# Kernel tuning notes

Measured on AMD Instinct MI355X. Metric: run time of the kernel, lower is better.

## Reference

```python
import jax, jax.numpy as jnp
import numpy as np

SESSION_CHANNELS = [128, 160, 192, 224, 240, 248, 252, 256]  # per-session channel counts
N_SESS = len(SESSION_CHANNELS)
B, MAX_C, MAX_T = 16, 256, 4096
HID, N_SRC = 512, 256


def setup_inputs() -> dict:
    key = jax.random.key(0)
    ks = jax.random.split(key, 7)
    session_ids = jax.random.randint(ks[0], (B,), 0, N_SESS)
    chan_table = jnp.asarray(SESSION_CHANNELS)
    channel_counts = chan_table[session_ids]
    seq_lens = jax.random.randint(ks[1], (B,), MAX_T // 2, MAX_T + 1)
    x = jax.random.normal(ks[2], (B, MAX_C, MAX_T), jnp.float32)
    # zero-pad beyond true channels and true time (as the docstring states)
    cmask = (jnp.arange(MAX_C)[None, :] < channel_counts[:, None]).astype(x.dtype)
    tmask = (jnp.arange(MAX_T)[None, :] < seq_lens[:, None]).astype(x.dtype)
    x = x * cmask[:, :, None] * tmask[:, None, :]
    # per-session Linear(num_channels -> HID), padded to MAX_C rows (torch-style uniform init)
    lim1 = 1.0 / np.sqrt(MAX_C)
    W_sess = jax.random.uniform(ks[3], (N_SESS, MAX_C, HID), jnp.float32, -lim1, lim1)
    b_sess = jax.random.uniform(ks[4], (N_SESS, HID), jnp.float32, -lim1, lim1)
    lim2 = 1.0 / np.sqrt(HID)
    W2 = jax.random.uniform(ks[5], (HID, N_SRC), jnp.float32, -lim2, lim2)
    b2 = jax.random.uniform(ks[6], (N_SRC,), jnp.float32, -lim2, lim2)
    return dict(x=x, session_ids=session_ids, channel_counts=channel_counts,
                seq_lens=seq_lens, W_sess=W_sess, b_sess=b_sess, W2=W2, b2=b2)


def reference(x, session_ids, channel_counts, seq_lens, W_sess, b_sess, W2, b2):
    # mask padded channels so the full-width contraction equals the sliced per-sample matmul
    cmask = (jnp.arange(x.shape[1])[None, :] < channel_counts[:, None]).astype(x.dtype)
    xm = x * cmask[:, :, None]                       # (B, Max_C, Max_T)
    W = W_sess[session_ids]                          # (B, Max_C, HID) gathered per sample
    b = b_sess[session_ids]                          # (B, HID)
    h = jnp.einsum('bct,bch->bht', xm, W) + b[:, :, None]
    h = jax.nn.gelu(h, approximate=False)            # torch nn.GELU default is exact erf
    out = jnp.einsum('bht,hs->bst', h, W2) + b2[None, :, None]  # (B, N_SRC, Max_T)
    tmask = (jnp.arange(x.shape[2])[None, :] < seq_lens[:, None]).astype(x.dtype)
    return out * tmask[:, None, :]
```

## Files before the change

### kernel.cpp

```cpp
#include <hip/hip_runtime.h>

typedef __attribute__((ext_vector_type(8))) _Float16 f16x8;
typedef __attribute__((ext_vector_type(4))) _Float16 f16x4;
typedef __attribute__((ext_vector_type(4))) float f32x4;

#define NB 16
#define MAXC 256
#define MAXT 4096
#define HID 512
#define NSRC 256
#define TT 64

__device__ __forceinline__ float gelu_fast(float x) {
  float p = x * x;
  float q = __builtin_fmaf(p, -0.10294336f, -2.30220778f);
  float e = __builtin_amdgcn_exp2f(x * q);
  return x * __builtin_amdgcn_rcpf(1.0f + e);
}

__global__ void transpose_cvt_kernel(const float* __restrict__ src,
                                     _Float16* __restrict__ dst, int R, int C) {
  __shared__ float tile[32][33];
  const float* s = src + (size_t)blockIdx.z * R * C;
  _Float16* d = dst + (size_t)blockIdx.z * R * C;
  int c0 = blockIdx.x * 32, r0 = blockIdx.y * 32;
  int tx = threadIdx.x, ty = threadIdx.y;
  for (int i = ty; i < 32; i += 8)
    tile[i][tx] = s[(size_t)(r0 + i) * C + (c0 + tx)];
  __syncthreads();
  for (int i = ty; i < 32; i += 8)
    d[(size_t)(c0 + i) * R + (r0 + tx)] = (_Float16)tile[tx][i];
}

__global__ __launch_bounds__(512, 4)
void fused_sess_proj_kernel(const float* __restrict__ x,
                            const int* __restrict__ sess_ids,
                            const int* __restrict__ seq_lens,
                            const _Float16* __restrict__ W1t,
                            const float* __restrict__ b_sess,
                            const _Float16* __restrict__ W2t,
                            const float* __restrict__ b2,
                            float* __restrict__ out) {
  int wg = blockIdx.x;
  int b = wg >> 6;
  int t0 = (wg & 63) * TT;
  int seqlen = seq_lens[b];
  int tid = threadIdx.x;

  if (t0 >= seqlen) {
    int row = tid >> 1;
    int part = tid & 1;
    float* po = out + ((size_t)b * NSRC + row) * MAXT + t0 + part * 32;
    f32x4 z = {0.f, 0.f, 0.f, 0.f};
    #pragma unroll
    for (int i = 0; i < 8; ++i) *(f32x4*)(po + i * 4) = z;
    return;
  }

  __shared__ _Float16 Xs[TT * MAXC];
  __shared__ _Float16 Hs[TT * 256];

  {
    int c = tid & 255;
    int th = tid >> 8;
    const float* xp = x + ((size_t)b * MAXC + c) * MAXT + t0 + th * 32;
    #pragma unroll
    for (int i = 0; i < 8; ++i) {
      f32x4 v = *(const f32x4*)(xp + i * 4);
      #pragma unroll
      for (int k = 0; k < 4; ++k) {
        int t = th * 32 + i * 4 + k;
        Xs[t * 256 + (c ^ ((t & 7) << 3))] = (_Float16)v[k];
      }
    }
  }
  __syncthreads();

  int lane = tid & 63;
  int w = tid >> 6;
  int lg = lane >> 4;
  int lr = lane & 15;
  int sid = sess_ids[b];
  const _Float16* W1s = W1t + (size_t)sid * HID * MAXC;

  f32x4 acc2[2][4];
  #pragma unroll
  for (int mi = 0; mi < 2; ++mi) {
    f32x4 bv = *(const f32x4*)(b2 + w * 32 + mi * 16 + lg * 4);
    #pragma unroll
    for (int ni = 0; ni < 4; ++ni) acc2[mi][ni] = bv;
  }

  #pragma unroll
  for (int ch = 0; ch < 2; ++ch) {
    f32x4 acc1[2][4];
    #pragma unroll
    for (int mi = 0; mi < 2; ++mi) {
      f32x4 bv = *(const f32x4*)(b_sess + sid * HID + ch * 256 + w * 32 + mi * 16 + lg * 4);
      #pragma unroll
      for (int ni = 0; ni < 4; ++ni) acc1[mi][ni] = bv;
    }
    #pragma unroll
    for (int ks = 0; ks < 8; ++ks) {
      int k0 = ks * 32;
      f16x8 af[2], bf[4];
      #pragma unroll
      for (int mi = 0; mi < 2; ++mi)
        af[mi] = *(const f16x8*)(W1s +
            (size_t)(ch * 256 + w * 32 + mi * 16 + lr) * MAXC + k0 + lg * 8);
      #pragma unroll
      for (int ni = 0; ni < 4; ++ni) {
        int t = ni * 16 + lr;
        bf[ni] = *(const f16x8*)(&Xs[t * 256 + ((k0 + lg * 8) ^ ((t & 7) << 3))]);
      }
      #pragma unroll
      for (int mi = 0; mi < 2; ++mi)
        #pragma unroll
        for (int ni = 0; ni < 4; ++ni)
          acc1[mi][ni] = __builtin_amdgcn_mfma_f32_16x16x32_f16(af[mi], bf[ni], acc1[mi][ni], 0, 0, 0);
    }
    #pragma unroll
    for (int mi = 0; mi < 2; ++mi) {
      int hh = w * 32 + mi * 16 + lg * 4;
      #pragma unroll
      for (int ni = 0; ni < 4; ++ni) {
        int t = ni * 16 + lr;
        f16x4 g;
        #pragma unroll
        for (int r = 0; r < 4; ++r) g[r] = (_Float16)gelu_fast(acc1[mi][ni][r]);
        *(f16x4*)(&Hs[t * 256 + (hh ^ ((t & 7) << 3))]) = g;
      }
    }
    __syncthreads();
    #pragma unroll
    for (int ks = 0; ks < 8; ++ks) {
      int k0 = ks * 32;
      f16x8 af[2], bf[4];
      #pragma unroll
      for (int mi = 0; mi < 2; ++mi)
        af[mi] = *(const f16x8*)(W2t +
            (size_t)(w * 32 + mi * 16 + lr) * HID + ch * 256 + k0 + lg * 8);
      #pragma unroll
      for (int ni = 0; ni < 4; ++ni) {
        int t = ni * 16 + lr;
        bf[ni] = *(const f16x8*)(&Hs[t * 256 + ((k0 + lg * 8) ^ ((t & 7) << 3))]);
      }
      #pragma unroll
      for (int mi = 0; mi < 2; ++mi)
        #pragma unroll
        for (int ni = 0; ni < 4; ++ni)
          acc2[mi][ni] = __builtin_amdgcn_mfma_f32_16x16x32_f16(af[mi], bf[ni], acc2[mi][ni], 0, 0, 0);
    }
    __syncthreads();
  }

  #pragma unroll
  for (int mi = 0; mi < 2; ++mi) {
    int s0 = w * 32 + mi * 16 + lg * 4;
    #pragma unroll
    for (int ni = 0; ni < 4; ++ni) {
      int t = t0 + ni * 16 + lr;
      float m = (t < seqlen) ? 1.0f : 0.0f;
      #pragma unroll
      for (int r = 0; r < 4; ++r)
        out[((size_t)b * NSRC + s0 + r) * MAXT + t] = acc2[mi][ni][r] * m;
    }
  }
}

extern "C" void kernel_launch(void* const* d_in, const int* in_sizes, int n_in,
                              void* d_out, int out_size, void* d_ws, size_t ws_size,
                              hipStream_t stream) {
  const float* x      = (const float*)d_in[0];
  const int* sess     = (const int*)d_in[1];
  const int* seq      = (const int*)d_in[3];
  const float* W_sess = (const float*)d_in[4];
  const float* b_sess = (const float*)d_in[5];
  const float* W2     = (const float*)d_in[6];
  const float* b2     = (const float*)d_in[7];
  float* out = (float*)d_out;

  _Float16* W1t = (_Float16*)d_ws;
  _Float16* W2t = (_Float16*)((char*)d_ws + (size_t)8 * HID * MAXC * sizeof(_Float16));

  dim3 tb(32, 8);
  transpose_cvt_kernel<<<dim3(HID / 32, MAXC / 32, 8), tb, 0, stream>>>(W_sess, W1t, MAXC, HID);
  transpose_cvt_kernel<<<dim3(NSRC / 32, HID / 32, 1), tb, 0, stream>>>(W2, W2t, HID, NSRC);

  fused_sess_proj_kernel<<<dim3(NB * (MAXT / TT)), dim3(512), 0, stream>>>(
      x, sess, seq, W1t, b_sess, W2t, b2, out);
}
```

Baseline: 90.30 us.

## Preload weight fragments into registers and interleave GEMM stages with double-buffered H

Holds all W1 and W2 A-fragments for the current half in registers, issuing those loads before the x tile staging. The next half's fragments are loaded while the current MFMAs run. The second half of GEMM1 is interleaved with the first half of GEMM2 using a double-buffered Hs, which removes one barrier and hides global weight latency. The cost is much higher register pressure (launch bounds lowered to 2 blocks per SM, with 64 extra VGPRs of fragments) and double the LDS for Hs, which cuts occupancy.

```diff
diff --git a/kernel.cpp b/kernel.cpp
--- a/kernel.cpp
+++ b/kernel.cpp
@@ -32,7 +32,7 @@
     d[(size_t)(c0 + i) * R + (r0 + tx)] = (_Float16)tile[tx][i];
 }
 
-__global__ __launch_bounds__(512, 4)
+__global__ __launch_bounds__(512, 2)
 void fused_sess_proj_kernel(const float* __restrict__ x,
                             const int* __restrict__ sess_ids,
                             const int* __restrict__ seq_lens,
@@ -58,23 +58,7 @@
   }
 
   __shared__ _Float16 Xs[TT * MAXC];
-  __shared__ _Float16 Hs[TT * 256];
-
-  {
-    int c = tid & 255;
-    int th = tid >> 8;
-    const float* xp = x + ((size_t)b * MAXC + c) * MAXT + t0 + th * 32;
-    #pragma unroll
-    for (int i = 0; i < 8; ++i) {
-      f32x4 v = *(const f32x4*)(xp + i * 4);
-      #pragma unroll
-      for (int k = 0; k < 4; ++k) {
-        int t = th * 32 + i * 4 + k;
-        Xs[t * 256 + (c ^ ((t & 7) << 3))] = (_Float16)v[k];
-      }
-    }
-  }
-  __syncthreads();
+  __shared__ _Float16 Hs[2][TT * 256];
 
   int lane = tid & 63;
   int w = tid >> 6;
@@ -83,31 +67,107 @@
   int sid = sess_ids[b];
   const _Float16* W1s = W1t + (size_t)sid * HID * MAXC;
 
-  f32x4 acc2[2][4];
-  #pragma unroll
-  for (int mi = 0; mi < 2; ++mi) {
-    f32x4 bv = *(const f32x4*)(b2 + w * 32 + mi * 16 + lg * 4);
-    #pragma unroll
-    for (int ni = 0; ni < 4; ++ni) acc2[mi][ni] = bv;
-  }
-
-  #pragma unroll
-  for (int ch = 0; ch < 2; ++ch) {
-    f32x4 acc1[2][4];
+  f16x8 AF1[8][2];
+  f16x8 AF2[8][2];
+  #pragma unroll
+  for (int ks = 0; ks < 8; ++ks)
     #pragma unroll
     for (int mi = 0; mi < 2; ++mi) {
-      f32x4 bv = *(const f32x4*)(b_sess + sid * HID + ch * 256 + w * 32 + mi * 16 + lg * 4);
-      #pragma unroll
-      for (int ni = 0; ni < 4; ++ni) acc1[mi][ni] = bv;
-    }
-    #pragma unroll
-    for (int ks = 0; ks < 8; ++ks) {
-      int k0 = ks * 32;
-      f16x8 af[2], bf[4];
+      AF1[ks][mi] = *(const f16x8*)(W1s +
+          (size_t)(w * 32 + mi * 16 + lr) * MAXC + ks * 32 + lg * 8);
+      AF2[ks][mi] = *(const f16x8*)(W2t +
+          (size_t)(w * 32 + mi * 16 + lr) * HID + ks * 32 + lg * 8);
+    }
+
+  {
+    int c = tid & 255;
+    int th = tid >> 8;
+    const float* xp = x + ((size_t)b * MAXC + c) * MAXT + t0 + th * 32;
+    #pragma unroll
+    for (int i = 0; i < 8; ++i) {
+      f32x4 v = *(const f32x4*)(xp + i * 4);
+      #pragma unroll
+      for (int k = 0; k < 4; ++k) {
+        int t = th * 32 + i * 4 + k;
+        Xs[t * 256 + (c ^ ((t & 7) << 3))] = (_Float16)v[k];
+      }
+    }
+  }
+
+  f32x4 acc2[2][4], acc1[2][4];
+  #pragma unroll
+  for (int mi = 0; mi < 2; ++mi) {
+    f32x4 bv2 = *(const f32x4*)(b2 + w * 32 + mi * 16 + lg * 4);
+    f32x4 bv1 = *(const f32x4*)(b_sess + sid * HID + w * 32 + mi * 16 + lg * 4);
+    #pragma unroll
+    for (int ni = 0; ni < 4; ++ni) { acc2[mi][ni] = bv2; acc1[mi][ni] = bv1; }
+  }
+
+  __syncthreads();
+
+  #pragma unroll
+  for (int ks = 0; ks < 8; ++ks) {
+    int k0 = ks * 32;
+    f16x8 bf[4];
+    #pragma unroll
+    for (int ni = 0; ni < 4; ++ni) {
+      int t = ni * 16 + lr;
+      bf[ni] = *(const f16x8*)(&Xs[t * 256 + ((k0 + lg * 8) ^ ((t & 7) << 3))]);
+    }
+    #pragma unroll
+    for (int mi = 0; mi < 2; ++mi)
+      #pragma unroll
+      for (int ni = 0; ni < 4; ++ni)
+        acc1[mi][ni] = __builtin_amdgcn_mfma_f32_16x16x32_f16(AF1[ks][mi], bf[ni], acc1[mi][ni], 0, 0, 0);
+    #pragma unroll
+    for (int mi = 0; mi < 2; ++mi)
+      AF1[ks][mi] = *(const f16x8*)(W1s +
+          (size_t)(256 + w * 32 + mi * 16 + lr) * MAXC + k0 + lg * 8);
+  }
+
+  #pragma unroll
+  for (int mi = 0; mi < 2; ++mi) {
+    int hh = w * 32 + mi * 16 + lg * 4;
+    #pragma unroll
+    for (int ni = 0; ni < 4; ++ni) {
+      int t = ni * 16 + lr;
+      f16x4 g;
+      #pragma unroll
+      for (int r = 0; r < 4; ++r) g[r] = (_Float16)gelu_fast(acc1[mi][ni][r]);
+      *(f16x4*)(&Hs[0][t * 256 + (hh ^ ((t & 7) << 3))]) = g;
+    }
+  }
+  #pragma unroll
+  for (int mi = 0; mi < 2; ++mi) {
+    f32x4 bv1 = *(const f32x4*)(b_sess + sid * HID + 256 + w * 32 + mi * 16 + lg * 4);
+    #pragma unroll
+    for (int ni = 0; ni < 4; ++ni) acc1[mi][ni] = bv1;
+  }
+
+  __syncthreads();
+
+  #pragma unroll
+  for (int ks = 0; ks < 8; ++ks) {
+    int k0 = ks * 32;
+    {
+      f16x8 bf[4];
+      #pragma unroll
+      for (int ni = 0; ni < 4; ++ni) {
+        int t = ni * 16 + lr;
+        bf[ni] = *(const f16x8*)(&Hs[0][t * 256 + ((k0 + lg * 8) ^ ((t & 7) << 3))]);
+      }
       #pragma unroll
       for (int mi = 0; mi < 2; ++mi)
-        af[mi] = *(const f16x8*)(W1s +
-            (size_t)(ch * 256 + w * 32 + mi * 16 + lr) * MAXC + k0 + lg * 8);
+        #pragma unroll
+        for (int ni = 0; ni < 4; ++ni)
+          acc2[mi][ni] = __builtin_amdgcn_mfma_f32_16x16x32_f16(AF2[ks][mi], bf[ni], acc2[mi][ni], 0, 0, 0);
+    }
+    #pragma unroll
+    for (int mi = 0; mi < 2; ++mi)
+      AF2[ks][mi] = *(const f16x8*)(W2t +
+          (size_t)(w * 32 + mi * 16 + lr) * HID + 256 + k0 + lg * 8);
+    {
+      f16x8 bf[4];
       #pragma unroll
       for (int ni = 0; ni < 4; ++ni) {
         int t = ni * 16 + lr;
@@ -117,41 +177,39 @@
       for (int mi = 0; mi < 2; ++mi)
         #pragma unroll
         for (int ni = 0; ni < 4; ++ni)
-          acc1[mi][ni] = __builtin_amdgcn_mfma_f32_16x16x32_f16(af[mi], bf[ni], acc1[mi][ni], 0, 0, 0);
-    }
-    #pragma unroll
-    for (int mi = 0; mi < 2; ++mi) {
-      int hh = w * 32 + mi * 16 + lg * 4;
-      #pragma unroll
-      for (int ni = 0; ni < 4; ++ni) {
-        int t = ni * 16 + lr;
-        f16x4 g;
-        #pragma unroll
-        for (int r = 0; r < 4; ++r) g[r] = (_Float16)gelu_fast(acc1[mi][ni][r]);
-        *(f16x4*)(&Hs[t * 256 + (hh ^ ((t & 7) << 3))]) = g;
-      }
-    }
-    __syncthreads();
-    #pragma unroll
-    for (int ks = 0; ks < 8; ++ks) {
-      int k0 = ks * 32;
-      f16x8 af[2], bf[4];
-      #pragma unroll
-      for (int mi = 0; mi < 2; ++mi)
-        af[mi] = *(const f16x8*)(W2t +
-            (size_t)(w * 32 + mi * 16 + lr) * HID + ch * 256 + k0 + lg * 8);
-      #pragma unroll
-      for (int ni = 0; ni < 4; ++ni) {
-        int t = ni * 16 + lr;
-        bf[ni] = *(const f16x8*)(&Hs[t * 256 + ((k0 + lg * 8) ^ ((t & 7) << 3))]);
-      }
-      #pragma unroll
-      for (int mi = 0; mi < 2; ++mi)
-        #pragma unroll
-        for (int ni = 0; ni < 4; ++ni)
-          acc2[mi][ni] = __builtin_amdgcn_mfma_f32_16x16x32_f16(af[mi], bf[ni], acc2[mi][ni], 0, 0, 0);
-    }
-    __syncthreads();
+          acc1[mi][ni] = __builtin_amdgcn_mfma_f32_16x16x32_f16(AF1[ks][mi], bf[ni], acc1[mi][ni], 0, 0, 0);
+    }
+  }
+
+  #pragma unroll
+  for (int mi = 0; mi < 2; ++mi) {
+    int hh = w * 32 + mi * 16 + lg * 4;
+    #pragma unroll
+    for (int ni = 0; ni < 4; ++ni) {
+      int t = ni * 16 + lr;
+      f16x4 g;
+      #pragma unroll
+      for (int r = 0; r < 4; ++r) g[r] = (_Float16)gelu_fast(acc1[mi][ni][r]);
+      *(f16x4*)(&Hs[1][t * 256 + (hh ^ ((t & 7) << 3))]) = g;
+    }
+  }
+
+  __syncthreads();
+
+  #pragma unroll
+  for (int ks = 0; ks < 8; ++ks) {
+    int k0 = ks * 32;
+    f16x8 bf[4];
+    #pragma unroll
+    for (int ni = 0; ni < 4; ++ni) {
+      int t = ni * 16 + lr;
+      bf[ni] = *(const f16x8*)(&Hs[1][t * 256 + ((k0 + lg * 8) ^ ((t & 7) << 3))]);
+    }
+    #pragma unroll
+    for (int mi = 0; mi < 2; ++mi)
+      #pragma unroll
+      for (int ni = 0; ni < 4; ++ni)
+        acc2[mi][ni] = __builtin_amdgcn_mfma_f32_16x16x32_f16(AF2[ks][mi], bf[ni], acc2[mi][ni], 0, 0, 0);
   }
 
   #pragma unroll
```

New measurement: 96.91 us. 1.07x slower.

## Double-buffer weight fragments in registers and restructure phases with lightweight barriers

Applied to the files above, without the earlier changes.

Unrolls the two hidden-dimension chunks into explicit phases. Each phase prefetches the next two k-steps of weight fragments into a register double buffer, so global weight loads overlap with MFMA work, and MFMA blocks are wrapped in s_setprio. Full __syncthreads are replaced by an inline-asm LDS-wait-plus-barrier. The second chunk's bias loads and weight prefetch are issued before the barrier. The x staging now has each thread load two channel rows and write packed fp16 pairs with cvt_pkrtz, which rounds toward zero instead of to nearest and so slightly changes numerics.

```diff
diff --git a/kernel.cpp b/kernel.cpp
--- a/kernel.cpp
+++ b/kernel.cpp
@@ -2,6 +2,7 @@
 
 typedef __attribute__((ext_vector_type(8))) _Float16 f16x8;
 typedef __attribute__((ext_vector_type(4))) _Float16 f16x4;
+typedef __attribute__((ext_vector_type(2))) __fp16 fp16v2;
 typedef __attribute__((ext_vector_type(4))) float f32x4;
 
 #define NB 16
@@ -10,6 +11,8 @@
 #define HID 512
 #define NSRC 256
 #define TT 64
+
+#define BAR() asm volatile("s_waitcnt lgkmcnt(0)\n\ts_barrier" ::: "memory")
 
 __device__ __forceinline__ float gelu_fast(float x) {
   float p = x * x;
@@ -31,6 +34,38 @@
   for (int i = ty; i < 32; i += 8)
     d[(size_t)(c0 + i) * R + (r0 + tx)] = (_Float16)tile[tx][i];
 }
+
+#define A1ADDR(mi, ks) (W1s + (size_t)(chbase + w * 32 + (mi)*16 + lr) * MAXC + (ks)*32 + lg * 8)
+#define A2ADDR(mi, ks) (W2t + (size_t)(w * 32 + (mi)*16 + lr) * HID + chbase + (ks)*32 + lg * 8)
+
+#define PREFETCH(AADDR)                          \
+  AF[0][0] = *(const f16x8*)AADDR(0, 0);         \
+  AF[0][1] = *(const f16x8*)AADDR(1, 0);         \
+  AF[1][0] = *(const f16x8*)AADDR(0, 1);         \
+  AF[1][1] = *(const f16x8*)AADDR(1, 1);
+
+#define RUN_PHASE(AADDR, BS, ACC)                                              \
+  _Pragma("unroll")                                                            \
+  for (int ks = 0; ks < 8; ++ks) {                                             \
+    f16x8 a0 = AF[ks & 1][0], a1 = AF[ks & 1][1];                              \
+    if (ks < 6) {                                                              \
+      AF[ks & 1][0] = *(const f16x8*)AADDR(0, ks + 2);                         \
+      AF[ks & 1][1] = *(const f16x8*)AADDR(1, ks + 2);                         \
+    }                                                                          \
+    f16x8 bf[4];                                                               \
+    _Pragma("unroll")                                                          \
+    for (int ni = 0; ni < 4; ++ni) {                                           \
+      int t = ni * 16 + lr;                                                    \
+      bf[ni] = *(const f16x8*)(&BS[t * 256 + ((ks * 32 + lg * 8) ^ ((t & 7) << 3))]); \
+    }                                                                          \
+    __builtin_amdgcn_s_setprio(1);                                             \
+    _Pragma("unroll")                                                          \
+    for (int ni = 0; ni < 4; ++ni) {                                           \
+      ACC[0][ni] = __builtin_amdgcn_mfma_f32_16x16x32_f16(a0, bf[ni], ACC[0][ni], 0, 0, 0); \
+      ACC[1][ni] = __builtin_amdgcn_mfma_f32_16x16x32_f16(a1, bf[ni], ACC[1][ni], 0, 0, 0); \
+    }                                                                          \
+    __builtin_amdgcn_s_setprio(0);                                             \
+  }
 
 __global__ __launch_bounds__(512, 4)
 void fused_sess_proj_kernel(const float* __restrict__ x,
@@ -60,22 +95,6 @@
   __shared__ _Float16 Xs[TT * MAXC];
   __shared__ _Float16 Hs[TT * 256];
 
-  {
-    int c = tid & 255;
-    int th = tid >> 8;
-    const float* xp = x + ((size_t)b * MAXC + c) * MAXT + t0 + th * 32;
-    #pragma unroll
-    for (int i = 0; i < 8; ++i) {
-      f32x4 v = *(const f32x4*)(xp + i * 4);
-      #pragma unroll
-      for (int k = 0; k < 4; ++k) {
-        int t = th * 32 + i * 4 + k;
-        Xs[t * 256 + (c ^ ((t & 7) << 3))] = (_Float16)v[k];
-      }
-    }
-  }
-  __syncthreads();
-
   int lane = tid & 63;
   int w = tid >> 6;
   int lg = lane >> 4;
@@ -83,76 +102,87 @@
   int sid = sess_ids[b];
   const _Float16* W1s = W1t + (size_t)sid * HID * MAXC;
 
-  f32x4 acc2[2][4];
-  #pragma unroll
-  for (int mi = 0; mi < 2; ++mi) {
-    f32x4 bv = *(const f32x4*)(b2 + w * 32 + mi * 16 + lg * 4);
-    #pragma unroll
-    for (int ni = 0; ni < 4; ++ni) acc2[mi][ni] = bv;
-  }
-
-  #pragma unroll
-  for (int ch = 0; ch < 2; ++ch) {
-    f32x4 acc1[2][4];
-    #pragma unroll
-    for (int mi = 0; mi < 2; ++mi) {
-      f32x4 bv = *(const f32x4*)(b_sess + sid * HID + ch * 256 + w * 32 + mi * 16 + lg * 4);
+  {
+    int c2 = (tid & 127) * 2;
+    int th = tid >> 7;
+    const float* xp = x + ((size_t)b * MAXC + c2) * MAXT + t0 + th * 16;
+    f32x4 va[4], vb[4];
+    #pragma unroll
+    for (int i = 0; i < 4; ++i) va[i] = *(const f32x4*)(xp + i * 4);
+    #pragma unroll
+    for (int i = 0; i < 4; ++i) vb[i] = *(const f32x4*)(xp + MAXT + i * 4);
+    #pragma unroll
+    for (int k = 0; k < 16; ++k) {
+      int t = th * 16 + k;
+      fp16v2 p = __builtin_amdgcn_cvt_pkrtz(va[k >> 2][k & 3], vb[k >> 2][k & 3]);
+      *(fp16v2*)(&Xs[t * 256 + (c2 ^ ((t & 7) << 3))]) = p;
+    }
+  }
+
+  f16x8 AF[2][2];
+  int chbase = 0;
+  PREFETCH(A1ADDR);
+
+  f32x4 acc2[2][4], acc1[2][4];
+  #pragma unroll
+  for (int mi = 0; mi < 2; ++mi) {
+    f32x4 bv2 = *(const f32x4*)(b2 + w * 32 + mi * 16 + lg * 4);
+    f32x4 bv1 = *(const f32x4*)(b_sess + sid * HID + w * 32 + mi * 16 + lg * 4);
+    #pragma unroll
+    for (int ni = 0; ni < 4; ++ni) { acc2[mi][ni] = bv2; acc1[mi][ni] = bv1; }
+  }
+
+  BAR();
+
+  RUN_PHASE(A1ADDR, Xs, acc1);
+
+  #pragma unroll
+  for (int mi = 0; mi < 2; ++mi) {
+    int hh = w * 32 + mi * 16 + lg * 4;
+    #pragma unroll
+    for (int ni = 0; ni < 4; ++ni) {
+      int t = ni * 16 + lr;
+      f16x4 g;
       #pragma unroll
-      for (int ni = 0; ni < 4; ++ni) acc1[mi][ni] = bv;
-    }
-    #pragma unroll
-    for (int ks = 0; ks < 8; ++ks) {
-      int k0 = ks * 32;
-      f16x8 af[2], bf[4];
+      for (int r = 0; r < 4; ++r) g[r] = (_Float16)gelu_fast(acc1[mi][ni][r]);
+      *(f16x4*)(&Hs[t * 256 + (hh ^ ((t & 7) << 3))]) = g;
+    }
+  }
+  #pragma unroll
+  for (int mi = 0; mi < 2; ++mi) {
+    f32x4 bv1 = *(const f32x4*)(b_sess + sid * HID + 256 + w * 32 + mi * 16 + lg * 4);
+    #pragma unroll
+    for (int ni = 0; ni < 4; ++ni) acc1[mi][ni] = bv1;
+  }
+
+  PREFETCH(A2ADDR);
+  BAR();
+
+  RUN_PHASE(A2ADDR, Hs, acc2);
+
+  chbase = 256;
+  PREFETCH(A1ADDR);
+  BAR();
+
+  RUN_PHASE(A1ADDR, Xs, acc1);
+
+  #pragma unroll
+  for (int mi = 0; mi < 2; ++mi) {
+    int hh = w * 32 + mi * 16 + lg * 4;
+    #pragma unroll
+    for (int ni = 0; ni < 4; ++ni) {
+      int t = ni * 16 + lr;
+      f16x4 g;
       #pragma unroll
-      for (int mi = 0; mi < 2; ++mi)
-        af[mi] = *(const f16x8*)(W1s +
-            (size_t)(ch * 256 + w * 32 + mi * 16 + lr) * MAXC + k0 + lg * 8);
-      #pragma unroll
-      for (int ni = 0; ni < 4; ++ni) {
-        int t = ni * 16 + lr;
-        bf[ni] = *(const f16x8*)(&Xs[t * 256 + ((k0 + lg * 8) ^ ((t & 7) << 3))]);
-      }
-      #pragma unroll
-      for (int mi = 0; mi < 2; ++mi)
-        #pragma unroll
-        for (int ni = 0; ni < 4; ++ni)
-          acc1[mi][ni] = __builtin_amdgcn_mfma_f32_16x16x32_f16(af[mi], bf[ni], acc1[mi][ni], 0, 0, 0);
-    }
-    #pragma unroll
-    for (int mi = 0; mi < 2; ++mi) {
-      int hh = w * 32 + mi * 16 + lg * 4;
-      #pragma unroll
-      for (int ni = 0; ni < 4; ++ni) {
-        int t = ni * 16 + lr;
-        f16x4 g;
-        #pragma unroll
-        for (int r = 0; r < 4; ++r) g[r] = (_Float16)gelu_fast(acc1[mi][ni][r]);
-        *(f16x4*)(&Hs[t * 256 + (hh ^ ((t & 7) << 3))]) = g;
-      }
-    }
-    __syncthreads();
-    #pragma unroll
-    for (int ks = 0; ks < 8; ++ks) {
-      int k0 = ks * 32;
-      f16x8 af[2], bf[4];
-      #pragma unroll
-      for (int mi = 0; mi < 2; ++mi)
-        af[mi] = *(const f16x8*)(W2t +
-            (size_t)(w * 32 + mi * 16 + lr) * HID + ch * 256 + k0 + lg * 8);
-      #pragma unroll
-      for (int ni = 0; ni < 4; ++ni) {
-        int t = ni * 16 + lr;
-        bf[ni] = *(const f16x8*)(&Hs[t * 256 + ((k0 + lg * 8) ^ ((t & 7) << 3))]);
-      }
-      #pragma unroll
-      for (int mi = 0; mi < 2; ++mi)
-        #pragma unroll
-        for (int ni = 0; ni < 4; ++ni)
-          acc2[mi][ni] = __builtin_amdgcn_mfma_f32_16x16x32_f16(af[mi], bf[ni], acc2[mi][ni], 0, 0, 0);
-    }
-    __syncthreads();
-  }
+      for (int r = 0; r < 4; ++r) g[r] = (_Float16)gelu_fast(acc1[mi][ni][r]);
+      *(f16x4*)(&Hs[t * 256 + (hh ^ ((t & 7) << 3))]) = g;
+    }
+  }
+
+  PREFETCH(A2ADDR);
+  BAR();
+
+  RUN_PHASE(A2ADDR, Hs, acc2);
 
   #pragma unroll
   for (int mi = 0; mi < 2; ++mi) {
```

Result: slower. 94.37 us (+4.5%).

## Make fused kernel persistent over four time tiles with prefetched x and weights

Applied to the files above, without the earlier changes.

Each workgroup now handles four consecutive 64-step time tiles, so the grid shrinks to 256 blocks. The next tile's x values are prefetched into registers while the current one is computed. Weight fragments are double-buffered from global memory. The full 512-wide hidden tile is kept in LDS, so the two hidden chunks and their extra barriers go away, and wave tiling is changed (4x4 for GEMM1, 4x2 for GEMM2). This aims to hide global load latency and cut per-block overhead, at the cost of more LDS and registers, lower occupancy, and fewer blocks to balance across CUs.

```diff
diff --git a/kernel.cpp b/kernel.cpp
--- a/kernel.cpp
+++ b/kernel.cpp
@@ -2,6 +2,7 @@
 
 typedef __attribute__((ext_vector_type(8))) _Float16 f16x8;
 typedef __attribute__((ext_vector_type(4))) _Float16 f16x4;
+typedef __attribute__((ext_vector_type(2))) __fp16 fp16v2;
 typedef __attribute__((ext_vector_type(4))) float f32x4;
 
 #define NB 16
@@ -10,6 +11,10 @@
 #define HID 512
 #define NSRC 256
 #define TT 64
+
+#define BAR() asm volatile("s_waitcnt lgkmcnt(0)\n\ts_barrier" ::: "memory")
+
+#define MFMA(a, b, c) __builtin_amdgcn_mfma_f32_16x16x32_f16(a, b, c, 0, 0, 0)
 
 __device__ __forceinline__ float gelu_fast(float x) {
   float p = x * x;
@@ -32,7 +37,7 @@
     d[(size_t)(c0 + i) * R + (r0 + tx)] = (_Float16)tile[tx][i];
 }
 
-__global__ __launch_bounds__(512, 4)
+__global__ __launch_bounds__(512, 2)
 void fused_sess_proj_kernel(const float* __restrict__ x,
                             const int* __restrict__ sess_ids,
                             const int* __restrict__ seq_lens,
@@ -41,129 +46,169 @@
                             const _Float16* __restrict__ W2t,
                             const float* __restrict__ b2,
                             float* __restrict__ out) {
-  int wg = blockIdx.x;
-  int b = wg >> 6;
-  int t0 = (wg & 63) * TT;
+  int g = blockIdx.x;
+  int b = g >> 4;
+  int tile0 = (g & 15) * 4;
   int seqlen = seq_lens[b];
+  int sid = sess_ids[b];
   int tid = threadIdx.x;
-
-  if (t0 >= seqlen) {
-    int row = tid >> 1;
-    int part = tid & 1;
-    float* po = out + ((size_t)b * NSRC + row) * MAXT + t0 + part * 32;
-    f32x4 z = {0.f, 0.f, 0.f, 0.f};
-    #pragma unroll
-    for (int i = 0; i < 8; ++i) *(f32x4*)(po + i * 4) = z;
-    return;
-  }
-
-  __shared__ _Float16 Xs[TT * MAXC];
-  __shared__ _Float16 Hs[TT * 256];
-
-  {
-    int c = tid & 255;
-    int th = tid >> 8;
-    const float* xp = x + ((size_t)b * MAXC + c) * MAXT + t0 + th * 32;
-    #pragma unroll
-    for (int i = 0; i < 8; ++i) {
-      f32x4 v = *(const f32x4*)(xp + i * 4);
-      #pragma unroll
-      for (int k = 0; k < 4; ++k) {
-        int t = th * 32 + i * 4 + k;
-        Xs[t * 256 + (c ^ ((t & 7) << 3))] = (_Float16)v[k];
-      }
-    }
-  }
-  __syncthreads();
-
   int lane = tid & 63;
   int w = tid >> 6;
   int lg = lane >> 4;
   int lr = lane & 15;
-  int sid = sess_ids[b];
+  int sb = w >> 1;
+  int tb = w & 1;
   const _Float16* W1s = W1t + (size_t)sid * HID * MAXC;
 
-  f32x4 acc2[2][4];
-  #pragma unroll
-  for (int mi = 0; mi < 2; ++mi) {
-    f32x4 bv = *(const f32x4*)(b2 + w * 32 + mi * 16 + lg * 4);
+  __shared__ _Float16 Xs[TT * MAXC];
+  __shared__ _Float16 Hs[TT * HID];
+
+  int c2 = (tid & 127) * 2;
+  int th = tid >> 7;
+  f32x4 va[4], vb[4];
+
+  bool act0 = (tile0 * TT) < seqlen;
+  if (act0) {
+    const float* xp = x + ((size_t)b * MAXC + c2) * MAXT + tile0 * TT + th * 16;
     #pragma unroll
-    for (int ni = 0; ni < 4; ++ni) acc2[mi][ni] = bv;
+    for (int i = 0; i < 4; ++i) va[i] = *(const f32x4*)(xp + i * 4);
+    #pragma unroll
+    for (int i = 0; i < 4; ++i) vb[i] = *(const f32x4*)(xp + MAXT + i * 4);
   }
 
-  #pragma unroll
-  for (int ch = 0; ch < 2; ++ch) {
-    f32x4 acc1[2][4];
-    #pragma unroll
-    for (int mi = 0; mi < 2; ++mi) {
-      f32x4 bv = *(const f32x4*)(b_sess + sid * HID + ch * 256 + w * 32 + mi * 16 + lg * 4);
-      #pragma unroll
-      for (int ni = 0; ni < 4; ++ni) acc1[mi][ni] = bv;
-    }
-    #pragma unroll
-    for (int ks = 0; ks < 8; ++ks) {
-      int k0 = ks * 32;
-      f16x8 af[2], bf[4];
-      #pragma unroll
-      for (int mi = 0; mi < 2; ++mi)
-        af[mi] = *(const f16x8*)(W1s +
-            (size_t)(ch * 256 + w * 32 + mi * 16 + lr) * MAXC + k0 + lg * 8);
-      #pragma unroll
-      for (int ni = 0; ni < 4; ++ni) {
-        int t = ni * 16 + lr;
-        bf[ni] = *(const f16x8*)(&Xs[t * 256 + ((k0 + lg * 8) ^ ((t & 7) << 3))]);
-      }
-      #pragma unroll
-      for (int mi = 0; mi < 2; ++mi)
-        #pragma unroll
-        for (int ni = 0; ni < 4; ++ni)
-          acc1[mi][ni] = __builtin_amdgcn_mfma_f32_16x16x32_f16(af[mi], bf[ni], acc1[mi][ni], 0, 0, 0);
-    }
-    #pragma unroll
-    for (int mi = 0; mi < 2; ++mi) {
-      int hh = w * 32 + mi * 16 + lg * 4;
-      #pragma unroll
-      for (int ni = 0; ni < 4; ++ni) {
-        int t = ni * 16 + lr;
-        f16x4 g;
-        #pragma unroll
-        for (int r = 0; r < 4; ++r) g[r] = (_Float16)gelu_fast(acc1[mi][ni][r]);
-        *(f16x4*)(&Hs[t * 256 + (hh ^ ((t & 7) << 3))]) = g;
-      }
-    }
-    __syncthreads();
-    #pragma unroll
-    for (int ks = 0; ks < 8; ++ks) {
-      int k0 = ks * 32;
-      f16x8 af[2], bf[4];
-      #pragma unroll
-      for (int mi = 0; mi < 2; ++mi)
-        af[mi] = *(const f16x8*)(W2t +
-            (size_t)(w * 32 + mi * 16 + lr) * HID + ch * 256 + k0 + lg * 8);
-      #pragma unroll
-      for (int ni = 0; ni < 4; ++ni) {
-        int t = ni * 16 + lr;
-        bf[ni] = *(const f16x8*)(&Hs[t * 256 + ((k0 + lg * 8) ^ ((t & 7) << 3))]);
-      }
-      #pragma unroll
-      for (int mi = 0; mi < 2; ++mi)
-        #pragma unroll
-        for (int ni = 0; ni < 4; ++ni)
-          acc2[mi][ni] = __builtin_amdgcn_mfma_f32_16x16x32_f16(af[mi], bf[ni], acc2[mi][ni], 0, 0, 0);
-    }
-    __syncthreads();
-  }
-
-  #pragma unroll
-  for (int mi = 0; mi < 2; ++mi) {
-    int s0 = w * 32 + mi * 16 + lg * 4;
-    #pragma unroll
-    for (int ni = 0; ni < 4; ++ni) {
-      int t = t0 + ni * 16 + lr;
-      float m = (t < seqlen) ? 1.0f : 0.0f;
-      #pragma unroll
-      for (int r = 0; r < 4; ++r)
-        out[((size_t)b * NSRC + s0 + r) * MAXT + t] = acc2[mi][ni][r] * m;
+  f16x8 AF[2][4];
+
+  #pragma unroll 1
+  for (int it = 0; it < 4; ++it) {
+    int t0 = (tile0 + it) * TT;
+    bool act = t0 < seqlen;
+    bool actn = (it < 3) && (t0 + TT < seqlen);
+
+    f32x4 acc1[4][4];
+    if (act) {
+      #pragma unroll
+      for (int k = 0; k < 16; ++k) {
+        int t = th * 16 + k;
+        fp16v2 p = __builtin_amdgcn_cvt_pkrtz(va[k >> 2][k & 3], vb[k >> 2][k & 3]);
+        *(fp16v2*)(&Xs[t * 256 + (c2 ^ ((t & 7) << 3))]) = p;
+      }
+      if (actn) {
+        const float* xp = x + ((size_t)b * MAXC + c2) * MAXT + t0 + TT + th * 16;
+        #pragma unroll
+        for (int i = 0; i < 4; ++i) va[i] = *(const f32x4*)(xp + i * 4);
+        #pragma unroll
+        for (int i = 0; i < 4; ++i) vb[i] = *(const f32x4*)(xp + MAXT + i * 4);
+      }
+      #pragma unroll
+      for (int mi = 0; mi < 4; ++mi) {
+        AF[0][mi] = *(const f16x8*)(W1s + (size_t)(w * 64 + mi * 16 + lr) * MAXC + lg * 8);
+        AF[1][mi] = *(const f16x8*)(W1s + (size_t)(w * 64 + mi * 16 + lr) * MAXC + 32 + lg * 8);
+      }
+      #pragma unroll
+      for (int mi = 0; mi < 4; ++mi) {
+        f32x4 bv = *(const f32x4*)(b_sess + sid * HID + w * 64 + mi * 16 + lg * 4);
+        #pragma unroll
+        for (int ni = 0; ni < 4; ++ni) acc1[mi][ni] = bv;
+      }
+    }
+    BAR();
+
+    if (act) {
+      #pragma unroll
+      for (int ks = 0; ks < 8; ++ks) {
+        f16x8 a[4];
+        #pragma unroll
+        for (int mi = 0; mi < 4; ++mi) a[mi] = AF[ks & 1][mi];
+        if (ks < 6) {
+          #pragma unroll
+          for (int mi = 0; mi < 4; ++mi)
+            AF[ks & 1][mi] = *(const f16x8*)(W1s +
+                (size_t)(w * 64 + mi * 16 + lr) * MAXC + (ks + 2) * 32 + lg * 8);
+        }
+        f16x8 bf[4];
+        #pragma unroll
+        for (int ni = 0; ni < 4; ++ni) {
+          int t = ni * 16 + lr;
+          bf[ni] = *(const f16x8*)(&Xs[t * 256 + ((ks * 32 + lg * 8) ^ ((t & 7) << 3))]);
+        }
+        #pragma unroll
+        for (int mi = 0; mi < 4; ++mi)
+          #pragma unroll
+          for (int ni = 0; ni < 4; ++ni)
+            acc1[mi][ni] = MFMA(a[mi], bf[ni], acc1[mi][ni]);
+      }
+      #pragma unroll
+      for (int mi = 0; mi < 4; ++mi) {
+        int hh = w * 64 + mi * 16 + lg * 4;
+        #pragma unroll
+        for (int ni = 0; ni < 4; ++ni) {
+          int t = ni * 16 + lr;
+          f16x4 gv;
+          #pragma unroll
+          for (int r = 0; r < 4; ++r) gv[r] = (_Float16)gelu_fast(acc1[mi][ni][r]);
+          *(f16x4*)(&Hs[t * 512 + (hh ^ ((t & 7) << 3))]) = gv;
+        }
+      }
+    }
+    f32x4 acc2[4][2];
+    if (act) {
+      #pragma unroll
+      for (int mi = 0; mi < 4; ++mi) {
+        AF[0][mi] = *(const f16x8*)(W2t + (size_t)(sb * 64 + mi * 16 + lr) * HID + lg * 8);
+        AF[1][mi] = *(const f16x8*)(W2t + (size_t)(sb * 64 + mi * 16 + lr) * HID + 32 + lg * 8);
+      }
+      #pragma unroll
+      for (int mi = 0; mi < 4; ++mi) {
+        f32x4 bv = *(const f32x4*)(b2 + sb * 64 + mi * 16 + lg * 4);
+        acc2[mi][0] = bv;
+        acc2[mi][1] = bv;
+      }
+    }
+    BAR();
+
+    if (act) {
+      #pragma unroll
+      for (int ks = 0; ks < 16; ++ks) {
+        f16x8 a[4];
+        #pragma unroll
+        for (int mi = 0; mi < 4; ++mi) a[mi] = AF[ks & 1][mi];
+        if (ks < 14) {
+          #pragma unroll
+          for (int mi = 0; mi < 4; ++mi)
+            AF[ks & 1][mi] = *(const f16x8*)(W2t +
+                (size_t)(sb * 64 + mi * 16 + lr) * HID + (ks + 2) * 32 + lg * 8);
+        }
+        f16x8 bf[2];
+        #pragma unroll
+        for (int ni = 0; ni < 2; ++ni) {
+          int t = tb * 32 + ni * 16 + lr;
+          bf[ni] = *(const f16x8*)(&Hs[t * 512 + ((ks * 32 + lg * 8) ^ ((t & 7) << 3))]);
+        }
+        #pragma unroll
+        for (int mi = 0; mi < 4; ++mi)
+          #pragma unroll
+          for (int ni = 0; ni < 2; ++ni)
+            acc2[mi][ni] = MFMA(a[mi], bf[ni], acc2[mi][ni]);
+      }
+      #pragma unroll
+      for (int mi = 0; mi < 4; ++mi) {
+        int s0 = sb * 64 + mi * 16 + lg * 4;
+        #pragma unroll
+        for (int ni = 0; ni < 2; ++ni) {
+          int t = t0 + tb * 32 + ni * 16 + lr;
+          float m = (t < seqlen) ? 1.0f : 0.0f;
+          #pragma unroll
+          for (int r = 0; r < 4; ++r)
+            out[((size_t)b * NSRC + s0 + r) * MAXT + t] = acc2[mi][ni][r] * m;
+        }
+      }
+    } else {
+      int row = tid >> 1;
+      int part = tid & 1;
+      float* po = out + ((size_t)b * NSRC + row) * MAXT + t0 + part * 32;
+      f32x4 z = {0.f, 0.f, 0.f, 0.f};
+      #pragma unroll
+      for (int i = 0; i < 8; ++i) *(f32x4*)(po + i * 4) = z;
     }
   }
 }
@@ -187,6 +232,6 @@
   transpose_cvt_kernel<<<dim3(HID / 32, MAXC / 32, 8), tb, 0, stream>>>(W_sess, W1t, MAXC, HID);
   transpose_cvt_kernel<<<dim3(NSRC / 32, HID / 32, 1), tb, 0, stream>>>(W2, W2t, HID, NSRC);
 
-  fused_sess_proj_kernel<<<dim3(NB * (MAXT / TT)), dim3(512), 0, stream>>>(
+  fused_sess_proj_kernel<<<dim3(256), dim3(512), 0, stream>>>(
       x, sess, seq, W1t, b_sess, W2t, b2, out);
 }
```

Result: slower. 187.0 us (+107.1%).
